# Kernel optimization log

Hardware: AMD Instinct MI355X
Metric: run time of the kernel (lower is better)

## Reference

```python
import jax, jax.numpy as jnp
import numpy as np

N_NODES = 50000
N_EDGES = 800000
IN_F = 128
HID = 64
H1 = 4  # heads layer 1
H2 = 1  # heads layer 2
N_GRAPHS = 32
NEG_SLOPE = 0.2  # PyG GATConv default leaky_relu slope


def _glorot(key, shape):
    fan_in, fan_out = shape[0], shape[-1]
    scale = jnp.sqrt(6.0 / (fan_in + fan_out))
    return jax.random.uniform(key, shape, jnp.float32, -scale, scale)


def setup_inputs() -> dict:
    key = jax.random.key(0)
    ks = jax.random.split(key, 10)
    x = jax.random.normal(ks[0], (N_NODES, IN_F), jnp.float32)
    edge_index = jax.random.randint(ks[1], (2, N_EDGES), 0, N_NODES, jnp.int64)
    batch = jnp.sort(jax.random.randint(ks[2], (N_NODES,), 0, N_GRAPHS, jnp.int64))
    # GATConv layer 1: in 128 -> 4 heads x 64, concat
    W1 = _glorot(ks[3], (IN_F, H1 * HID))
    a_src1 = _glorot(ks[4], (H1, HID))
    a_dst1 = _glorot(ks[5], (H1, HID))
    b1 = jnp.zeros((H1 * HID,), jnp.float32)
    # GATConv layer 2: in 256 -> 1 head x 64
    W2 = _glorot(ks[6], (H1 * HID, H2 * HID))
    a_src2 = _glorot(ks[7], (H2, HID))
    a_dst2 = _glorot(ks[8], (H2, HID))
    b2 = jnp.zeros((H2 * HID,), jnp.float32)
    return {"x": x, "edge_index": edge_index, "batch": batch,
            "W1": W1, "a_src1": a_src1, "a_dst1": a_dst1, "b1": b1,
            "W2": W2, "a_src2": a_src2, "a_dst2": a_dst2, "b2": b2}


def gat_layer(x, src, dst, W, a_src, a_dst, bias, num_nodes):
    """PyG-style GATConv with concat=True output [N, H*C]."""
    H, C = a_src.shape
    h = (x @ W).reshape(num_nodes, H, C)            # [N,H,C]
    alpha_src = jnp.sum(h * a_src[None], axis=-1)   # [N,H]
    alpha_dst = jnp.sum(h * a_dst[None], axis=-1)   # [N,H]
    e = jax.nn.leaky_relu(alpha_src[src] + alpha_dst[dst], NEG_SLOPE)  # [E,H]
    # segment softmax over destination neighborhoods
    m = jax.ops.segment_max(e, dst, num_segments=num_nodes)
    ex = jnp.exp(e - m[dst])
    denom = jax.ops.segment_sum(ex, dst, num_segments=num_nodes)
    alpha = ex / (denom[dst] + 1e-16)               # [E,H]
    out = jax.ops.segment_sum(h[src] * alpha[:, :, None], dst, num_segments=num_nodes)
    return out.reshape(num_nodes, H * C) + bias


def reference(x, edge_index, batch, W1, a_src1, a_dst1, b1, W2, a_src2, a_dst2, b2):
    N = x.shape[0]
    # PyG GATConv adds self-loops by default
    loops = jnp.arange(N, dtype=edge_index.dtype)
    src = jnp.concatenate([edge_index[0], loops])
    dst = jnp.concatenate([edge_index[1], loops])
    h = jax.nn.relu(gat_layer(x, src, dst, W1, a_src1, a_dst1, b1, N))
    h = gat_layer(h, src, dst, W2, a_src2, a_dst2, b2, N)
    # role == 'global': global mean pool over batch ids
    sums = jax.ops.segment_sum(h, batch, num_segments=N_GRAPHS)
    cnt = jax.ops.segment_sum(jnp.ones((N, 1), h.dtype), batch, num_segments=N_GRAPHS)
    return sums / jnp.maximum(cnt, 1.0)
```

## Files before the change

kernel.cpp:

```cpp
#include <hip/hip_runtime.h>
#include <cmath>

#define HID 64
typedef unsigned short ushort_t;
typedef __attribute__((ext_vector_type(8))) short bf16x8;
typedef __attribute__((ext_vector_type(4))) float f32x4;

__device__ inline ushort_t f2b(float f) {
    unsigned u = __float_as_uint(f);
    unsigned r = (u + 0x7fffu + ((u >> 16) & 1u)) >> 16;
    return (ushort_t)r;
}
__device__ inline float b2f(ushort_t b) { return __uint_as_float(((unsigned)b) << 16); }


__global__ void fill_f32(float* __restrict__ p, float v, long n) {
    long i = (long)blockIdx.x * blockDim.x + threadIdx.x;
    long stride = (long)gridDim.x * blockDim.x;
    for (; i < n; i += stride) p[i] = v;
}

__global__ void fill_i32(int* __restrict__ p, int v, long n) {
    long i = (long)blockIdx.x * blockDim.x + threadIdx.x;
    long stride = (long)gridDim.x * blockDim.x;
    for (; i < n; i += stride) p[i] = v;
}

__global__ __launch_bounds__(256) void transp_both(const float* __restrict__ W1,
                                                   const float* __restrict__ W2,
                                                   ushort_t* __restrict__ W1t,
                                                   ushort_t* __restrict__ W2t) {
    int b = blockIdx.x;
    int t = threadIdx.x;
    if (b < 128) {
        W1t[(size_t)t * 128 + b] = f2b(W1[(size_t)b * 256 + t]);
    } else {
        int k = b - 128;
        if (t < 64)
            W2t[(size_t)t * 256 + k] = f2b(W2[(size_t)k * 64 + t]);
    }
}

template<int WM, int WN, int K, bool AF32, bool B_WHOLE, int AH>
__global__ __launch_bounds__(WM * WN * 64) void gemm_mfma(
        const void* __restrict__ Ap, const ushort_t* __restrict__ Bt,
        ushort_t* __restrict__ Cb, const float* __restrict__ a_src,
        const float* __restrict__ a_dst, float* __restrict__ os,
        float* __restrict__ od, int M) {
    constexpr int T = WM * WN * 64;
    constexpr int BM = WM * 64;
    constexpr int BN = WN * 64;
    constexpr int BSTR = B_WHOLE ? (K + 8) : 40;

    __shared__ ushort_t Alds[BM][40];
    __shared__ ushort_t Blds[BN][BSTR];

    const int tid = threadIdx.x;
    const int bm = blockIdx.x * BM;
    const int w = tid >> 6;
    const int l = tid & 63;
    const int lr = l >> 4;
    const int lc = l & 15;
    const int row0 = (WM == 1) ? 0 : w * 64;
    const int col0 = (WN == 1) ? 0 : w * 64;

    f32x4 acc[4][4] = {};

    if (B_WHOLE) {
        constexpr int UPR = K / 8;
        for (int u = tid; u < BN * UPR; u += T) {
            int row = u / UPR, j = u % UPR;
            *(bf16x8*)&Blds[row][j * 8] = *(const bf16x8*)&Bt[(size_t)row * K + j * 8];
        }
    }

    for (int kk = 0; kk < K / 32; ++kk) {
        __syncthreads();
        for (int u = tid; u < BM * 4; u += T) {
            int row = u >> 2, part = u & 3;
            int gm = bm + row;
            bf16x8 v = {0, 0, 0, 0, 0, 0, 0, 0};
            if (gm < M) {
                if (AF32) {
                    const float* ap = (const float*)Ap + (size_t)gm * K + kk * 32 + part * 8;
                    float4 v0 = *(const float4*)ap;
                    float4 v1 = *(const float4*)(ap + 4);
                    v[0] = (short)f2b(v0.x); v[1] = (short)f2b(v0.y);
                    v[2] = (short)f2b(v0.z); v[3] = (short)f2b(v0.w);
                    v[4] = (short)f2b(v1.x); v[5] = (short)f2b(v1.y);
                    v[6] = (short)f2b(v1.z); v[7] = (short)f2b(v1.w);
                } else {
                    v = *(const bf16x8*)((const ushort_t*)Ap + (size_t)gm * K + kk * 32 + part * 8);
                }
            }
            *(bf16x8*)&Alds[row][part * 8] = v;
        }
        if (!B_WHOLE) {
            for (int u = tid; u < BN * 4; u += T) {
                int col = u >> 2, part = u & 3;
                *(bf16x8*)&Blds[col][part * 8] =
                    *(const bf16x8*)&Bt[(size_t)col * K + kk * 32 + part * 8];
            }
        }
        __syncthreads();

        const int koff = B_WHOLE ? kk * 32 : 0;
        bf16x8 af[4], bfr[4];
        #pragma unroll
        for (int fr = 0; fr < 4; ++fr)
            af[fr] = *(const bf16x8*)&Alds[row0 + fr * 16 + lc][lr * 8];
        #pragma unroll
        for (int fc = 0; fc < 4; ++fc)
            bfr[fc] = *(const bf16x8*)&Blds[col0 + fc * 16 + lc][koff + lr * 8];
        #pragma unroll
        for (int fr = 0; fr < 4; ++fr)
            #pragma unroll
            for (int fc = 0; fc < 4; ++fc)
                acc[fr][fc] = __builtin_amdgcn_mfma_f32_16x16x32_bf16(
                    af[fr], bfr[fc], acc[fr][fc], 0, 0, 0);
    }

    #pragma unroll
    for (int fr = 0; fr < 4; ++fr)
        #pragma unroll
        for (int r = 0; r < 4; ++r) {
            int gm = bm + row0 + fr * 16 + lr * 4 + r;
            if (gm >= M) continue;
            #pragma unroll
            for (int fc = 0; fc < 4; ++fc)
                Cb[(size_t)gm * BN + col0 + fc * 16 + lc] = f2b(acc[fr][fc][r]);
        }

    if (AH > 0) {
        const int head = (WN > 1) ? w : 0;
        const float* __restrict__ asv = a_src + head * 64;
        const float* __restrict__ adv = a_dst + head * 64;
        #pragma unroll
        for (int fr = 0; fr < 4; ++fr)
            #pragma unroll
            for (int r = 0; r < 4; ++r) {
                float ps = 0.f, pd = 0.f;
                #pragma unroll
                for (int fc = 0; fc < 4; ++fc) {
                    float av = acc[fr][fc][r];
                    ps = fmaf(av, asv[fc * 16 + lc], ps);
                    pd = fmaf(av, adv[fc * 16 + lc], pd);
                }
                #pragma unroll
                for (int off = 1; off < 16; off <<= 1) {
                    ps += __shfl_xor(ps, off, 64);
                    pd += __shfl_xor(pd, off, 64);
                }
                int gm = bm + row0 + fr * 16 + lr * 4 + r;
                if (lc == 0 && gm < M) {
                    os[(size_t)gm * AH + head] = ps;
                    od[(size_t)gm * AH + head] = pd;
                }
            }
    }
}


__global__ void count_k(const int* __restrict__ ei, int E, int N, int* __restrict__ deg) {
    int e = blockIdx.x * blockDim.x + threadIdx.x;
    int T = E + N;
    if (e >= T) return;
    int d = (e < E) ? ei[E + e] : (e - E);
    atomicAdd(&deg[d], 1);
}

__global__ __launch_bounds__(256) void scan1_k(const int* __restrict__ deg,
                                               int* __restrict__ bsum, int N) {
    int i = blockIdx.x * 256 + threadIdx.x;
    int v = (i < N) ? deg[i] : 0;
    #pragma unroll
    for (int off = 32; off > 0; off >>= 1) v += __shfl_xor(v, off, 64);
    __shared__ int ws[4];
    if ((threadIdx.x & 63) == 0) ws[threadIdx.x >> 6] = v;
    __syncthreads();
    if (threadIdx.x == 0) bsum[blockIdx.x] = ws[0] + ws[1] + ws[2] + ws[3];
}

__global__ __launch_bounds__(256) void scan2_k(int* __restrict__ bsum, int nb) {
    int t = threadIdx.x;
    int lane = t & 63, wave = t >> 6;
    int v = (t < nb) ? bsum[t] : 0;
    int inc = v;
    #pragma unroll
    for (int off = 1; off < 64; off <<= 1) {
        int u = __shfl_up(inc, off, 64);
        if (lane >= off) inc += u;
    }
    __shared__ int wsum[4];
    if (lane == 63) wsum[wave] = inc;
    __syncthreads();
    int woff = 0;
    for (int w = 0; w < wave; ++w) woff += wsum[w];
    if (t < nb) bsum[t] = inc - v + woff;
}

__global__ __launch_bounds__(256) void scan3_k(const int* __restrict__ deg,
                                               const int* __restrict__ bsum,
                                               int* __restrict__ rowstart, int N) {
    int i = blockIdx.x * 256 + threadIdx.x;
    int lane = threadIdx.x & 63, wave = threadIdx.x >> 6;
    int v = (i < N) ? deg[i] : 0;
    int inc = v;
    #pragma unroll
    for (int off = 1; off < 64; off <<= 1) {
        int u = __shfl_up(inc, off, 64);
        if (lane >= off) inc += u;
    }
    __shared__ int wsum[4];
    if (lane == 63) wsum[wave] = inc;
    __syncthreads();
    int woff = bsum[blockIdx.x];
    for (int w = 0; w < wave; ++w) woff += wsum[w];
    int excl = inc - v + woff;
    if (i < N) rowstart[i] = excl;
    if (i == N - 1) rowstart[N] = excl + v;
}

__global__ void scatter_k(const int* __restrict__ ei, int E, int N,
                          const int* __restrict__ rowstart, int* __restrict__ cursor,
                          int* __restrict__ srcs) {
    int e = blockIdx.x * blockDim.x + threadIdx.x;
    int T = E + N;
    if (e >= T) return;
    int s, d;
    if (e < E) { s = ei[e]; d = ei[E + e]; } else { s = e - E; d = s; }
    int p = atomicAdd(&cursor[d], 1);
    srcs[rowstart[d] + p] = s;
}

#define MAXD 128
__global__ __launch_bounds__(256) void gat_agg4(const ushort_t* __restrict__ hb,
        const int* __restrict__ rowstart, const int* __restrict__ srcs,
        const float* __restrict__ as, const float* __restrict__ ad,
        const float* __restrict__ bias, ushort_t* __restrict__ outb, int N) {
    __shared__ int ssrc_s[4][MAXD];
    __shared__ float sw_s[4][MAXD][4];
    __shared__ float hstat_s[4][2][4];
    const int wave = threadIdx.x >> 6;
    const int lane = threadIdx.x & 63;
    int d = blockIdx.x * 4 + wave;
    if (d >= N) return;
    int* ssrc = ssrc_s[wave];
    float (*sw)[4] = sw_s[wave];
    int beg = rowstart[d];
    int deg = rowstart[d + 1] - beg;
    int dcap = deg < MAXD ? deg : MAXD;
    for (int i = lane; i < dcap; i += 64) ssrc[i] = srcs[beg + i];

    const int isub = lane >> 2;
    const int hd = lane & 3;
    float adv = ad[d * 4 + hd];
    float vmax = -INFINITY;
    for (int e0 = 0; e0 < deg; e0 += 16) {
        int e = e0 + isub;
        if (e < deg) {
            int s = (e < MAXD) ? ssrc[e] : srcs[beg + e];
            float v = as[s * 4 + hd] + adv;
            v = v > 0.f ? v : 0.2f * v;
            if (e < MAXD) sw[e][hd] = v;
            vmax = fmaxf(vmax, v);
        }
    }
    #pragma unroll
    for (int off = 4; off < 64; off <<= 1) vmax = fmaxf(vmax, __shfl_xor(vmax, off, 64));
    float dsum = 0.f;
    for (int e0 = 0; e0 < deg; e0 += 16) {
        int e = e0 + isub;
        if (e < deg) {
            float v;
            if (e < MAXD) v = sw[e][hd];
            else {
                int s = srcs[beg + e];
                v = as[s * 4 + hd] + adv;
                v = v > 0.f ? v : 0.2f * v;
            }
            float ex = __expf(v - vmax);
            if (e < MAXD) sw[e][hd] = ex;
            dsum += ex;
        }
    }
    #pragma unroll
    for (int off = 4; off < 64; off <<= 1) dsum += __shfl_xor(dsum, off, 64);
    float rden = 1.f / (dsum + 1e-16f);
    for (int e0 = 0; e0 < dcap; e0 += 16) {
        int e = e0 + isub;
        if (e < dcap) sw[e][hd] *= rden;
    }
    if (deg > MAXD && isub == 0) {
        hstat_s[wave][0][hd] = vmax;
        hstat_s[wave][1][hd] = rden;
    }

    const int hd2 = lane >> 4;
    const ushort_t* __restrict__ hrow = hb + (size_t)(lane * 4);
    float a0 = 0.f, a1 = 0.f, a2 = 0.f, a3 = 0.f;
    int e = 0;
    for (; e + 2 <= dcap; e += 2) {
        int s0 = __builtin_amdgcn_readfirstlane(ssrc[e]);
        int s1 = __builtin_amdgcn_readfirstlane(ssrc[e + 1]);
        float w0 = sw[e][hd2], w1 = sw[e + 1][hd2];
        ushort4 g0 = *(const ushort4*)(hrow + (size_t)s0 * 256);
        ushort4 g1 = *(const ushort4*)(hrow + (size_t)s1 * 256);
        a0 = fmaf(b2f(g0.x), w0, a0); a1 = fmaf(b2f(g0.y), w0, a1);
        a2 = fmaf(b2f(g0.z), w0, a2); a3 = fmaf(b2f(g0.w), w0, a3);
        a0 = fmaf(b2f(g1.x), w1, a0); a1 = fmaf(b2f(g1.y), w1, a1);
        a2 = fmaf(b2f(g1.z), w1, a2); a3 = fmaf(b2f(g1.w), w1, a3);
    }
    for (; e < dcap; ++e) {
        int s = __builtin_amdgcn_readfirstlane(ssrc[e]);
        float w = sw[e][hd2];
        ushort4 g = *(const ushort4*)(hrow + (size_t)s * 256);
        a0 = fmaf(b2f(g.x), w, a0); a1 = fmaf(b2f(g.y), w, a1);
        a2 = fmaf(b2f(g.z), w, a2); a3 = fmaf(b2f(g.w), w, a3);
    }
    if (deg > MAXD) {
        float vm2 = hstat_s[wave][0][hd2];
        float rd2 = hstat_s[wave][1][hd2];
        float adv2 = ad[d * 4 + hd2];
        for (int j = MAXD; j < deg; ++j) {
            int s = srcs[beg + j];
            float v = as[s * 4 + hd2] + adv2;
            v = v > 0.f ? v : 0.2f * v;
            float w = __expf(v - vm2) * rd2;
            ushort4 g = *(const ushort4*)(hrow + (size_t)s * 256);
            a0 = fmaf(b2f(g.x), w, a0); a1 = fmaf(b2f(g.y), w, a1);
            a2 = fmaf(b2f(g.z), w, a2); a3 = fmaf(b2f(g.w), w, a3);
        }
    }
    int cb = lane * 4;
    ushort4 ov;
    ov.x = f2b(fmaxf(a0 + bias[cb + 0], 0.f));
    ov.y = f2b(fmaxf(a1 + bias[cb + 1], 0.f));
    ov.z = f2b(fmaxf(a2 + bias[cb + 2], 0.f));
    ov.w = f2b(fmaxf(a3 + bias[cb + 3], 0.f));
    *(ushort4*)&outb[(size_t)d * 256 + cb] = ov;
}

__global__ __launch_bounds__(256) void gat_agg1(const ushort_t* __restrict__ hb,
        const int* __restrict__ rowstart, const int* __restrict__ srcs,
        const float* __restrict__ as, const float* __restrict__ ad,
        const float* __restrict__ bias, float* __restrict__ out2, int N) {
    __shared__ int ssrc_s[4][MAXD];
    __shared__ float sw_s[4][MAXD];
    const int wave = threadIdx.x >> 6;
    const int lane = threadIdx.x & 63;
    int d = blockIdx.x * 4 + wave;
    if (d >= N) return;
    int* ssrc = ssrc_s[wave];
    float* sw = sw_s[wave];
    int beg = rowstart[d];
    int deg = rowstart[d + 1] - beg;
    int dcap = deg < MAXD ? deg : MAXD;
    for (int i = lane; i < dcap; i += 64) ssrc[i] = srcs[beg + i];

    float adv = ad[d];
    float vmax = -INFINITY;
    for (int e0 = 0; e0 < deg; e0 += 64) {
        int e = e0 + lane;
        if (e < deg) {
            int s = (e < MAXD) ? ssrc[e] : srcs[beg + e];
            float v = as[s] + adv;
            v = v > 0.f ? v : 0.2f * v;
            if (e < MAXD) sw[e] = v;
            vmax = fmaxf(vmax, v);
        }
    }
    #pragma unroll
    for (int off = 1; off < 64; off <<= 1) vmax = fmaxf(vmax, __shfl_xor(vmax, off, 64));
    float dsum = 0.f;
    for (int e0 = 0; e0 < deg; e0 += 64) {
        int e = e0 + lane;
        if (e < deg) {
            float v;
            if (e < MAXD) v = sw[e];
            else {
                int s = srcs[beg + e];
                v = as[s] + adv;
                v = v > 0.f ? v : 0.2f * v;
            }
            float ex = __expf(v - vmax);
            if (e < MAXD) sw[e] = ex;
            dsum += ex;
        }
    }
    #pragma unroll
    for (int off = 1; off < 64; off <<= 1) dsum += __shfl_xor(dsum, off, 64);
    float rden = 1.f / (dsum + 1e-16f);
    for (int e0 = 0; e0 < dcap; e0 += 64) {
        int e = e0 + lane;
        if (e < dcap) sw[e] *= rden;
    }

    const int esub = lane >> 4;
    const int cg = lane & 15;
    const ushort_t* __restrict__ hrow = hb + (size_t)(cg * 4);
    float a0 = 0.f, a1 = 0.f, a2 = 0.f, a3 = 0.f;
    int e0 = 0;
    for (; e0 + 4 <= dcap; e0 += 4) {
        int e = e0 + esub;
        int s = ssrc[e];
        float w = sw[e];
        ushort4 g = *(const ushort4*)(hrow + (size_t)s * 64);
        a0 = fmaf(b2f(g.x), w, a0); a1 = fmaf(b2f(g.y), w, a1);
        a2 = fmaf(b2f(g.z), w, a2); a3 = fmaf(b2f(g.w), w, a3);
    }
    if (e0 < dcap) {
        int e = e0 + esub;
        if (e < dcap) {
            int s = ssrc[e];
            float w = sw[e];
            ushort4 g = *(const ushort4*)(hrow + (size_t)s * 64);
            a0 = fmaf(b2f(g.x), w, a0); a1 = fmaf(b2f(g.y), w, a1);
            a2 = fmaf(b2f(g.z), w, a2); a3 = fmaf(b2f(g.w), w, a3);
        }
    }
    for (int j = MAXD + esub; j < deg; j += 4) {
        int s = srcs[beg + j];
        float v = as[s] + adv;
        v = v > 0.f ? v : 0.2f * v;
        float w = __expf(v - vmax) * rden;
        ushort4 g = *(const ushort4*)(hrow + (size_t)s * 64);
        a0 = fmaf(b2f(g.x), w, a0); a1 = fmaf(b2f(g.y), w, a1);
        a2 = fmaf(b2f(g.z), w, a2); a3 = fmaf(b2f(g.w), w, a3);
    }
    a0 += __shfl_xor(a0, 16, 64); a0 += __shfl_xor(a0, 32, 64);
    a1 += __shfl_xor(a1, 16, 64); a1 += __shfl_xor(a1, 32, 64);
    a2 += __shfl_xor(a2, 16, 64); a2 += __shfl_xor(a2, 32, 64);
    a3 += __shfl_xor(a3, 16, 64); a3 += __shfl_xor(a3, 32, 64);
    if (esub == 0) {
        int cb = cg * 4;
        float4 o;
        o.x = a0 + bias[cb + 0];
        o.y = a1 + bias[cb + 1];
        o.z = a2 + bias[cb + 2];
        o.w = a3 + bias[cb + 3];
        *(float4*)&out2[(size_t)d * 64 + cb] = o;
    }
}

__global__ void pool_k(const float* __restrict__ h, const int* __restrict__ batch,
                       float* __restrict__ pool, float* __restrict__ cnt, int N) {
    const int NPB = 128;
    int c = threadIdx.x;
    int start = blockIdx.x * NPB;
    int end = min(start + NPB, N);
    float acc = 0.f;
    float cl = 0.f;
    int cur = -1;
    for (int n = start; n < end; ++n) {
        int b = batch[n];
        if (b != cur) {
            if (cur >= 0) {
                atomicAdd(&pool[cur * HID + c], acc);
                if (c == 0) atomicAdd(&cnt[cur], cl);
            }
            cur = b; acc = 0.f; cl = 0.f;
        }
        acc += h[(size_t)n * HID + c];
        cl += 1.f;
    }
    if (cur >= 0) {
        atomicAdd(&pool[cur * HID + c], acc);
        if (c == 0) atomicAdd(&cnt[cur], cl);
    }
}

__global__ void finalize_k(const float* __restrict__ pool, const float* __restrict__ cnt,
                           float* __restrict__ out) {
    int g = blockIdx.x;
    int c = threadIdx.x;
    out[g * HID + c] = pool[g * HID + c] / fmaxf(cnt[g], 1.f);
}


extern "C" void kernel_launch(void* const* d_in, const int* in_sizes, int n_in,
                              void* d_out, int out_size, void* d_ws, size_t ws_size,
                              hipStream_t stream) {
    const float* x      = (const float*)d_in[0];
    const int*   ei     = (const int*)d_in[1];
    const int*   batch  = (const int*)d_in[2];
    const float* W1     = (const float*)d_in[3];
    const float* a_src1 = (const float*)d_in[4];
    const float* a_dst1 = (const float*)d_in[5];
    const float* b1     = (const float*)d_in[6];
    const float* W2     = (const float*)d_in[7];
    const float* a_src2 = (const float*)d_in[8];
    const float* a_dst2 = (const float*)d_in[9];
    const float* b2     = (const float*)d_in[10];
    float* out = (float*)d_out;

    const int N = in_sizes[0] / 128;
    const int E = in_sizes[1] / 2;
    const int F1 = 256;
    const int F2 = 64;
    const int NG = 32;
    const int T = E + N;
    const int NB = (N + 255) / 256;

    float* ws = (float*)d_ws;
    size_t o = 0;
    ushort_t* h1b   = (ushort_t*)(ws + o); o += (size_t)N * F1 / 2;
    ushort_t* out1b = (ushort_t*)(ws + o); o += (size_t)N * F1 / 2;
    ushort_t* h2b   = (ushort_t*)(ws + o); o += (size_t)N * F2 / 2;
    float* out2  = ws + o; o += (size_t)N * F2;
    float* asrc1 = ws + o; o += (size_t)N * 4;
    float* adst1 = ws + o; o += (size_t)N * 4;
    float* asrc2 = ws + o; o += (size_t)N;
    float* adst2 = ws + o; o += (size_t)N;
    float* pools = ws + o; o += (size_t)NG * HID;
    float* cnts  = ws + o; o += (size_t)NG;
    ushort_t* W1t = (ushort_t*)(ws + o); o += 256 * 128 / 2;
    ushort_t* W2t = (ushort_t*)(ws + o); o += 64 * 256 / 2;
    int* ib = (int*)(ws + o);
    size_t io = 0;
    int* deg      = ib + io; io += N;
    int* cursor   = ib + io; io += N;
    int* rowstart = ib + io; io += N + 1;
    int* bsum     = ib + io; io += NB;
    int* srcs     = ib + io; io += T;
    (void)ws_size; (void)n_in; (void)out_size;

    transp_both<<<384, 256, 0, stream>>>(W1, W2, W1t, W2t);

    fill_i32<<<256, 256, 0, stream>>>(deg, 0, 2L * N);
    count_k<<<(T + 255) / 256, 256, 0, stream>>>(ei, E, N, deg);
    scan1_k<<<NB, 256, 0, stream>>>(deg, bsum, N);
    scan2_k<<<1, 256, 0, stream>>>(bsum, NB);
    scan3_k<<<NB, 256, 0, stream>>>(deg, bsum, rowstart, N);
    scatter_k<<<(T + 255) / 256, 256, 0, stream>>>(ei, E, N, rowstart, cursor, srcs);

    gemm_mfma<1, 4, 128, true, false, 4><<<(N + 63) / 64, 256, 0, stream>>>(
        x, W1t, h1b, a_src1, a_dst1, asrc1, adst1, N);
    gat_agg4<<<(N + 3) / 4, 256, 0, stream>>>(h1b, rowstart, srcs, asrc1, adst1, b1, out1b, N);

    gemm_mfma<2, 1, 256, false, true, 1><<<(N + 127) / 128, 128, 0, stream>>>(
        out1b, W2t, h2b, a_src2, a_dst2, asrc2, adst2, N);
    gat_agg1<<<(N + 3) / 4, 256, 0, stream>>>(h2b, rowstart, srcs, asrc2, adst2, b2, out2, N);

    fill_f32<<<8, 256, 0, stream>>>(pools, 0.f, (long)NG * HID + NG);
    pool_k<<<(N + 127) / 128, 64, 0, stream>>>(out2, batch, pools, cnts, N);
    finalize_k<<<NG, HID, 0, stream>>>(pools, cnts, out);
}
```

Baseline: 287.4 us.

## Fuse mean pooling into layer-2 aggregation and merge scan and prep kernels

Layer-2 aggregation now scales each node row by the reciprocal of its graph's node count and atomically accumulates into the output. This removes the intermediate feature buffer and the pool and finalize kernels. Graph counts and output zeroing move into the weight-transpose prep kernel. The single-block scan pass is folded into the final scan, and the layer-1 gather loop is unrolled to four edges. Contention on the output atomics is the trade-off, and float atomics make summation order nondeterministic.

After: 256.1 us. 10.9% less time.

```diff
diff --git a/kernel.cpp b/kernel.cpp
--- a/kernel.cpp
+++ b/kernel.cpp
@@ -14,30 +14,39 @@
 __device__ inline float b2f(ushort_t b) { return __uint_as_float(((unsigned)b) << 16); }
 
 
-__global__ void fill_f32(float* __restrict__ p, float v, long n) {
-    long i = (long)blockIdx.x * blockDim.x + threadIdx.x;
-    long stride = (long)gridDim.x * blockDim.x;
-    for (; i < n; i += stride) p[i] = v;
-}
-
 __global__ void fill_i32(int* __restrict__ p, int v, long n) {
     long i = (long)blockIdx.x * blockDim.x + threadIdx.x;
     long stride = (long)gridDim.x * blockDim.x;
     for (; i < n; i += stride) p[i] = v;
 }
 
-__global__ __launch_bounds__(256) void transp_both(const float* __restrict__ W1,
-                                                   const float* __restrict__ W2,
-                                                   ushort_t* __restrict__ W1t,
-                                                   ushort_t* __restrict__ W2t) {
+__global__ __launch_bounds__(256) void prep_k(const float* __restrict__ W1,
+                                              const float* __restrict__ W2,
+                                              ushort_t* __restrict__ W1t,
+                                              ushort_t* __restrict__ W2t,
+                                              const int* __restrict__ batch,
+                                              int* __restrict__ cnt_i,
+                                              float* __restrict__ outp,
+                                              int N, int NHB) {
     int b = blockIdx.x;
     int t = threadIdx.x;
     if (b < 128) {
         W1t[(size_t)t * 128 + b] = f2b(W1[(size_t)b * 256 + t]);
+    } else if (b < 384) {
+        int k = b - 128;
+        if (t < 64) W2t[(size_t)t * 256 + k] = f2b(W2[(size_t)k * 64 + t]);
+    } else if (b < 384 + NHB) {
+        __shared__ int lh[32];
+        if (t < 32) lh[t] = 0;
+        __syncthreads();
+        int i = (b - 384) * 256 + t;
+        if (i < N) atomicAdd(&lh[batch[i]], 1);
+        __syncthreads();
+        if (t < 32 && lh[t] > 0) atomicAdd(&cnt_i[t], lh[t]);
     } else {
-        int k = b - 128;
-        if (t < 64)
-            W2t[(size_t)t * 256 + k] = f2b(W2[(size_t)k * 64 + t]);
+        int i = t * 8;
+        #pragma unroll
+        for (int j = 0; j < 8; ++j) outp[i + j] = 0.f;
     }
 }
 
@@ -181,29 +190,20 @@
     if (threadIdx.x == 0) bsum[blockIdx.x] = ws[0] + ws[1] + ws[2] + ws[3];
 }
 
-__global__ __launch_bounds__(256) void scan2_k(int* __restrict__ bsum, int nb) {
+__global__ __launch_bounds__(256) void scan3_k(const int* __restrict__ deg,
+                                               const int* __restrict__ bsum,
+                                               int* __restrict__ rowstart, int N, int NB) {
     int t = threadIdx.x;
     int lane = t & 63, wave = t >> 6;
-    int v = (t < nb) ? bsum[t] : 0;
-    int inc = v;
+    int pv = (t < NB && t < (int)blockIdx.x) ? bsum[t] : 0;
     #pragma unroll
-    for (int off = 1; off < 64; off <<= 1) {
-        int u = __shfl_up(inc, off, 64);
-        if (lane >= off) inc += u;
-    }
-    __shared__ int wsum[4];
-    if (lane == 63) wsum[wave] = inc;
+    for (int off = 32; off > 0; off >>= 1) pv += __shfl_xor(pv, off, 64);
+    __shared__ int wsp[4];
+    if (lane == 0) wsp[wave] = pv;
     __syncthreads();
-    int woff = 0;
-    for (int w = 0; w < wave; ++w) woff += wsum[w];
-    if (t < nb) bsum[t] = inc - v + woff;
-}
-
-__global__ __launch_bounds__(256) void scan3_k(const int* __restrict__ deg,
-                                               const int* __restrict__ bsum,
-                                               int* __restrict__ rowstart, int N) {
-    int i = blockIdx.x * 256 + threadIdx.x;
-    int lane = threadIdx.x & 63, wave = threadIdx.x >> 6;
+    int base = wsp[0] + wsp[1] + wsp[2] + wsp[3];
+
+    int i = blockIdx.x * 256 + t;
     int v = (i < N) ? deg[i] : 0;
     int inc = v;
     #pragma unroll
@@ -214,7 +214,7 @@
     __shared__ int wsum[4];
     if (lane == 63) wsum[wave] = inc;
     __syncthreads();
-    int woff = bsum[blockIdx.x];
+    int woff = base;
     for (int w = 0; w < wave; ++w) woff += wsum[w];
     int excl = inc - v + woff;
     if (i < N) rowstart[i] = excl;
@@ -300,16 +300,25 @@
     const ushort_t* __restrict__ hrow = hb + (size_t)(lane * 4);
     float a0 = 0.f, a1 = 0.f, a2 = 0.f, a3 = 0.f;
     int e = 0;
-    for (; e + 2 <= dcap; e += 2) {
+    for (; e + 4 <= dcap; e += 4) {
         int s0 = __builtin_amdgcn_readfirstlane(ssrc[e]);
         int s1 = __builtin_amdgcn_readfirstlane(ssrc[e + 1]);
-        float w0 = sw[e][hd2], w1 = sw[e + 1][hd2];
+        int s2 = __builtin_amdgcn_readfirstlane(ssrc[e + 2]);
+        int s3 = __builtin_amdgcn_readfirstlane(ssrc[e + 3]);
         ushort4 g0 = *(const ushort4*)(hrow + (size_t)s0 * 256);
         ushort4 g1 = *(const ushort4*)(hrow + (size_t)s1 * 256);
+        ushort4 g2 = *(const ushort4*)(hrow + (size_t)s2 * 256);
+        ushort4 g3 = *(const ushort4*)(hrow + (size_t)s3 * 256);
+        float w0 = sw[e][hd2], w1 = sw[e + 1][hd2];
+        float w2 = sw[e + 2][hd2], w3 = sw[e + 3][hd2];
         a0 = fmaf(b2f(g0.x), w0, a0); a1 = fmaf(b2f(g0.y), w0, a1);
         a2 = fmaf(b2f(g0.z), w0, a2); a3 = fmaf(b2f(g0.w), w0, a3);
         a0 = fmaf(b2f(g1.x), w1, a0); a1 = fmaf(b2f(g1.y), w1, a1);
         a2 = fmaf(b2f(g1.z), w1, a2); a3 = fmaf(b2f(g1.w), w1, a3);
+        a0 = fmaf(b2f(g2.x), w2, a0); a1 = fmaf(b2f(g2.y), w2, a1);
+        a2 = fmaf(b2f(g2.z), w2, a2); a3 = fmaf(b2f(g2.w), w2, a3);
+        a0 = fmaf(b2f(g3.x), w3, a0); a1 = fmaf(b2f(g3.y), w3, a1);
+        a2 = fmaf(b2f(g3.z), w3, a2); a3 = fmaf(b2f(g3.w), w3, a3);
     }
     for (; e < dcap; ++e) {
         int s = __builtin_amdgcn_readfirstlane(ssrc[e]);
@@ -344,137 +353,127 @@
 __global__ __launch_bounds__(256) void gat_agg1(const ushort_t* __restrict__ hb,
         const int* __restrict__ rowstart, const int* __restrict__ srcs,
         const float* __restrict__ as, const float* __restrict__ ad,
-        const float* __restrict__ bias, float* __restrict__ out2, int N) {
+        const float* __restrict__ bias, const int* __restrict__ batch,
+        const int* __restrict__ cnt_i, float* __restrict__ outp, int N) {
     __shared__ int ssrc_s[4][MAXD];
     __shared__ float sw_s[4][MAXD];
+    __shared__ float prow[4][64];
+    __shared__ int gws[4];
     const int wave = threadIdx.x >> 6;
     const int lane = threadIdx.x & 63;
     int d = blockIdx.x * 4 + wave;
-    if (d >= N) return;
-    int* ssrc = ssrc_s[wave];
-    float* sw = sw_s[wave];
-    int beg = rowstart[d];
-    int deg = rowstart[d + 1] - beg;
-    int dcap = deg < MAXD ? deg : MAXD;
-    for (int i = lane; i < dcap; i += 64) ssrc[i] = srcs[beg + i];
-
-    float adv = ad[d];
-    float vmax = -INFINITY;
-    for (int e0 = 0; e0 < deg; e0 += 64) {
-        int e = e0 + lane;
-        if (e < deg) {
-            int s = (e < MAXD) ? ssrc[e] : srcs[beg + e];
-            float v = as[s] + adv;
-            v = v > 0.f ? v : 0.2f * v;
-            if (e < MAXD) sw[e] = v;
-            vmax = fmaxf(vmax, v);
-        }
-    }
-    #pragma unroll
-    for (int off = 1; off < 64; off <<= 1) vmax = fmaxf(vmax, __shfl_xor(vmax, off, 64));
-    float dsum = 0.f;
-    for (int e0 = 0; e0 < deg; e0 += 64) {
-        int e = e0 + lane;
-        if (e < deg) {
-            float v;
-            if (e < MAXD) v = sw[e];
-            else {
-                int s = srcs[beg + e];
-                v = as[s] + adv;
+    bool active = d < N;
+    if (active) {
+        int* ssrc = ssrc_s[wave];
+        float* sw = sw_s[wave];
+        int beg = rowstart[d];
+        int deg = rowstart[d + 1] - beg;
+        int dcap = deg < MAXD ? deg : MAXD;
+        for (int i = lane; i < dcap; i += 64) ssrc[i] = srcs[beg + i];
+
+        float adv = ad[d];
+        float vmax = -INFINITY;
+        for (int e0 = 0; e0 < deg; e0 += 64) {
+            int e = e0 + lane;
+            if (e < deg) {
+                int s = (e < MAXD) ? ssrc[e] : srcs[beg + e];
+                float v = as[s] + adv;
                 v = v > 0.f ? v : 0.2f * v;
-            }
-            float ex = __expf(v - vmax);
-            if (e < MAXD) sw[e] = ex;
-            dsum += ex;
-        }
-    }
-    #pragma unroll
-    for (int off = 1; off < 64; off <<= 1) dsum += __shfl_xor(dsum, off, 64);
-    float rden = 1.f / (dsum + 1e-16f);
-    for (int e0 = 0; e0 < dcap; e0 += 64) {
-        int e = e0 + lane;
-        if (e < dcap) sw[e] *= rden;
-    }
-
-    const int esub = lane >> 4;
-    const int cg = lane & 15;
-    const ushort_t* __restrict__ hrow = hb + (size_t)(cg * 4);
-    float a0 = 0.f, a1 = 0.f, a2 = 0.f, a3 = 0.f;
-    int e0 = 0;
-    for (; e0 + 4 <= dcap; e0 += 4) {
-        int e = e0 + esub;
-        int s = ssrc[e];
-        float w = sw[e];
-        ushort4 g = *(const ushort4*)(hrow + (size_t)s * 64);
-        a0 = fmaf(b2f(g.x), w, a0); a1 = fmaf(b2f(g.y), w, a1);
-        a2 = fmaf(b2f(g.z), w, a2); a3 = fmaf(b2f(g.w), w, a3);
-    }
-    if (e0 < dcap) {
-        int e = e0 + esub;
-        if (e < dcap) {
+                if (e < MAXD) sw[e] = v;
+                vmax = fmaxf(vmax, v);
+            }
+        }
+        #pragma unroll
+        for (int off = 1; off < 64; off <<= 1) vmax = fmaxf(vmax, __shfl_xor(vmax, off, 64));
+        float dsum = 0.f;
+        for (int e0 = 0; e0 < deg; e0 += 64) {
+            int e = e0 + lane;
+            if (e < deg) {
+                float v;
+                if (e < MAXD) v = sw[e];
+                else {
+                    int s = srcs[beg + e];
+                    v = as[s] + adv;
+                    v = v > 0.f ? v : 0.2f * v;
+                }
+                float ex = __expf(v - vmax);
+                if (e < MAXD) sw[e] = ex;
+                dsum += ex;
+            }
+        }
+        #pragma unroll
+        for (int off = 1; off < 64; off <<= 1) dsum += __shfl_xor(dsum, off, 64);
+        float rden = 1.f / (dsum + 1e-16f);
+        for (int e0 = 0; e0 < dcap; e0 += 64) {
+            int e = e0 + lane;
+            if (e < dcap) sw[e] *= rden;
+        }
+
+        const int esub = lane >> 4;
+        const int cg = lane & 15;
+        const ushort_t* __restrict__ hrow = hb + (size_t)(cg * 4);
+        float a0 = 0.f, a1 = 0.f, a2 = 0.f, a3 = 0.f;
+        int e0 = 0;
+        for (; e0 + 4 <= dcap; e0 += 4) {
+            int e = e0 + esub;
             int s = ssrc[e];
             float w = sw[e];
             ushort4 g = *(const ushort4*)(hrow + (size_t)s * 64);
             a0 = fmaf(b2f(g.x), w, a0); a1 = fmaf(b2f(g.y), w, a1);
             a2 = fmaf(b2f(g.z), w, a2); a3 = fmaf(b2f(g.w), w, a3);
         }
-    }
-    for (int j = MAXD + esub; j < deg; j += 4) {
-        int s = srcs[beg + j];
-        float v = as[s] + adv;
-        v = v > 0.f ? v : 0.2f * v;
-        float w = __expf(v - vmax) * rden;
-        ushort4 g = *(const ushort4*)(hrow + (size_t)s * 64);
-        a0 = fmaf(b2f(g.x), w, a0); a1 = fmaf(b2f(g.y), w, a1);
-        a2 = fmaf(b2f(g.z), w, a2); a3 = fmaf(b2f(g.w), w, a3);
-    }
-    a0 += __shfl_xor(a0, 16, 64); a0 += __shfl_xor(a0, 32, 64);
-    a1 += __shfl_xor(a1, 16, 64); a1 += __shfl_xor(a1, 32, 64);
-    a2 += __shfl_xor(a2, 16, 64); a2 += __shfl_xor(a2, 32, 64);
-    a3 += __shfl_xor(a3, 16, 64); a3 += __shfl_xor(a3, 32, 64);
-    if (esub == 0) {
-        int cb = cg * 4;
-        float4 o;
-        o.x = a0 + bias[cb + 0];
-        o.y = a1 + bias[cb + 1];
-        o.z = a2 + bias[cb + 2];
-        o.w = a3 + bias[cb + 3];
-        *(float4*)&out2[(size_t)d * 64 + cb] = o;
-    }
-}
-
-__global__ void pool_k(const float* __restrict__ h, const int* __restrict__ batch,
-                       float* __restrict__ pool, float* __restrict__ cnt, int N) {
-    const int NPB = 128;
-    int c = threadIdx.x;
-    int start = blockIdx.x * NPB;
-    int end = min(start + NPB, N);
-    float acc = 0.f;
-    float cl = 0.f;
-    int cur = -1;
-    for (int n = start; n < end; ++n) {
-        int b = batch[n];
-        if (b != cur) {
-            if (cur >= 0) {
-                atomicAdd(&pool[cur * HID + c], acc);
-                if (c == 0) atomicAdd(&cnt[cur], cl);
-            }
-            cur = b; acc = 0.f; cl = 0.f;
-        }
-        acc += h[(size_t)n * HID + c];
-        cl += 1.f;
-    }
-    if (cur >= 0) {
-        atomicAdd(&pool[cur * HID + c], acc);
-        if (c == 0) atomicAdd(&cnt[cur], cl);
-    }
-}
-
-__global__ void finalize_k(const float* __restrict__ pool, const float* __restrict__ cnt,
-                           float* __restrict__ out) {
-    int g = blockIdx.x;
-    int c = threadIdx.x;
-    out[g * HID + c] = pool[g * HID + c] / fmaxf(cnt[g], 1.f);
+        if (e0 < dcap) {
+            int e = e0 + esub;
+            if (e < dcap) {
+                int s = ssrc[e];
+                float w = sw[e];
+                ushort4 g = *(const ushort4*)(hrow + (size_t)s * 64);
+                a0 = fmaf(b2f(g.x), w, a0); a1 = fmaf(b2f(g.y), w, a1);
+                a2 = fmaf(b2f(g.z), w, a2); a3 = fmaf(b2f(g.w), w, a3);
+            }
+        }
+        for (int j = MAXD + esub; j < deg; j += 4) {
+            int s = srcs[beg + j];
+            float v = as[s] + adv;
+            v = v > 0.f ? v : 0.2f * v;
+            float w = __expf(v - vmax) * rden;
+            ushort4 g = *(const ushort4*)(hrow + (size_t)s * 64);
+            a0 = fmaf(b2f(g.x), w, a0); a1 = fmaf(b2f(g.y), w, a1);
+            a2 = fmaf(b2f(g.z), w, a2); a3 = fmaf(b2f(g.w), w, a3);
+        }
+        a0 += __shfl_xor(a0, 16, 64); a0 += __shfl_xor(a0, 32, 64);
+        a1 += __shfl_xor(a1, 16, 64); a1 += __shfl_xor(a1, 32, 64);
+        a2 += __shfl_xor(a2, 16, 64); a2 += __shfl_xor(a2, 32, 64);
+        a3 += __shfl_xor(a3, 16, 64); a3 += __shfl_xor(a3, 32, 64);
+        int g = batch[d];
+        if (esub == 0) {
+            float cntf = fmaxf((float)cnt_i[g], 1.f);
+            float rc = 1.f / cntf;
+            int cb = cg * 4;
+            float4 o;
+            o.x = (a0 + bias[cb + 0]) * rc;
+            o.y = (a1 + bias[cb + 1]) * rc;
+            o.z = (a2 + bias[cb + 2]) * rc;
+            o.w = (a3 + bias[cb + 3]) * rc;
+            *(float4*)&prow[wave][cb] = o;
+        }
+        if (lane == 0) gws[wave] = g;
+    } else {
+        if (lane == 0) gws[wave] = -1;
+    }
+    __syncthreads();
+    if (threadIdx.x < 64) {
+        int t = threadIdx.x;
+        int g0 = gws[0];
+        if (g0 >= 0 && gws[1] == g0 && gws[2] == g0 && gws[3] == g0) {
+            atomicAdd(&outp[g0 * 64 + t],
+                      prow[0][t] + prow[1][t] + prow[2][t] + prow[3][t]);
+        } else {
+            #pragma unroll
+            for (int w2 = 0; w2 < 4; ++w2)
+                if (gws[w2] >= 0) atomicAdd(&outp[gws[w2] * 64 + t], prow[w2][t]);
+        }
+    }
 }
 
 
@@ -498,7 +497,6 @@
     const int E = in_sizes[1] / 2;
     const int F1 = 256;
     const int F2 = 64;
-    const int NG = 32;
     const int T = E + N;
     const int NB = (N + 255) / 256;
 
@@ -507,31 +505,28 @@
     ushort_t* h1b   = (ushort_t*)(ws + o); o += (size_t)N * F1 / 2;
     ushort_t* out1b = (ushort_t*)(ws + o); o += (size_t)N * F1 / 2;
     ushort_t* h2b   = (ushort_t*)(ws + o); o += (size_t)N * F2 / 2;
-    float* out2  = ws + o; o += (size_t)N * F2;
     float* asrc1 = ws + o; o += (size_t)N * 4;
     float* adst1 = ws + o; o += (size_t)N * 4;
     float* asrc2 = ws + o; o += (size_t)N;
     float* adst2 = ws + o; o += (size_t)N;
-    float* pools = ws + o; o += (size_t)NG * HID;
-    float* cnts  = ws + o; o += (size_t)NG;
     ushort_t* W1t = (ushort_t*)(ws + o); o += 256 * 128 / 2;
     ushort_t* W2t = (ushort_t*)(ws + o); o += 64 * 256 / 2;
     int* ib = (int*)(ws + o);
     size_t io = 0;
     int* deg      = ib + io; io += N;
     int* cursor   = ib + io; io += N;
+    int* cnt_i    = ib + io; io += 32;
     int* rowstart = ib + io; io += N + 1;
     int* bsum     = ib + io; io += NB;
     int* srcs     = ib + io; io += T;
     (void)ws_size; (void)n_in; (void)out_size;
 
-    transp_both<<<384, 256, 0, stream>>>(W1, W2, W1t, W2t);
-
-    fill_i32<<<256, 256, 0, stream>>>(deg, 0, 2L * N);
+    fill_i32<<<256, 256, 0, stream>>>(deg, 0, 2L * N + 32);
+    prep_k<<<384 + NB + 1, 256, 0, stream>>>(W1, W2, W1t, W2t, batch, cnt_i, out, N, NB);
+
     count_k<<<(T + 255) / 256, 256, 0, stream>>>(ei, E, N, deg);
     scan1_k<<<NB, 256, 0, stream>>>(deg, bsum, N);
-    scan2_k<<<1, 256, 0, stream>>>(bsum, NB);
-    scan3_k<<<NB, 256, 0, stream>>>(deg, bsum, rowstart, N);
+    scan3_k<<<NB, 256, 0, stream>>>(deg, bsum, rowstart, N, NB);
     scatter_k<<<(T + 255) / 256, 256, 0, stream>>>(ei, E, N, rowstart, cursor, srcs);
 
     gemm_mfma<1, 4, 128, true, false, 4><<<(N + 63) / 64, 256, 0, stream>>>(
@@ -540,9 +535,6 @@
 
     gemm_mfma<2, 1, 256, false, true, 1><<<(N + 127) / 128, 128, 0, stream>>>(
         out1b, W2t, h2b, a_src2, a_dst2, asrc2, adst2, N);
-    gat_agg1<<<(N + 3) / 4, 256, 0, stream>>>(h2b, rowstart, srcs, asrc2, adst2, b2, out2, N);
-
-    fill_f32<<<8, 256, 0, stream>>>(pools, 0.f, (long)NG * HID + NG);
-    pool_k<<<(N + 127) / 128, 64, 0, stream>>>(out2, batch, pools, cnts, N);
-    finalize_k<<<NG, HID, 0, stream>>>(pools, cnts, out);
-}
+    gat_agg1<<<(N + 3) / 4, 256, 0, stream>>>(h2b, rowstart, srcs, asrc2, adst2, b2,
+                                              batch, cnt_i, out, N);
+}
```
